# Kernel optimization log

Measured on AMD Instinct MI355X. Metric: run time of the kernel, lower is better.

The kernel has to match this reference:

```python
import jax, jax.numpy as jnp
import numpy as np
from jax import lax

B, N, C, CN, M, H, W = 2, 8192, 64, 64, 16, 180, 240
LN_EPS = 1e-5  # torch nn.LayerNorm([C]) default eps


def setup_inputs():
    key = jax.random.key(0)
    ks = jax.random.split(key, 20)
    x = jax.random.uniform(ks[0], (B, N)) * (W - 1)
    y = jax.random.uniform(ks[1], (B, N)) * (H - 1)
    t = jax.random.uniform(ks[2], (B, N))
    p = jnp.where(jax.random.uniform(ks[3], (B, N)) < 0.5, -1.0, 1.0)
    events = jnp.stack([x, y, t, p], axis=-1)  # [B,N,4]
    s = 0.05
    w = lambda k, shape: jax.random.normal(k, shape) * s
    return {
        "events": events,
        "W_mlp1": w(ks[4], (4, C)),
        "W_pe": w(ks[5], (4, CN)),
        "ln_w": jnp.ones((C,)),
        "ln_b": jnp.zeros((C,)),
        "lx_Wq": w(ks[6], (C, CN)), "lx_Wk": w(ks[7], (C, CN)),
        "lx_Wv": w(ks[8], (C, CN)), "lx_Wsa1": w(ks[9], (CN, 1)),
        "lx_Wsa2": w(ks[10], (CN, C)),
        "gx_Wq": w(ks[11], (C, CN)), "gx_Wk": w(ks[12], (C, CN)),
        "gx_Wv": w(ks[13], (C, CN)), "gx_Wpe": w(ks[14], (C, CN)),
        "gx_Wsa1": w(ks[15], (CN, 1)), "gx_Wsa2": w(ks[16], (CN, C)),
    }


def select_nearest(vect, m):
    # torch: F.pad(left=m//2, right=m//2-1) then unfold(dim=1, size=m, step=1)
    b, n, c = vect.shape
    pad = m // 2
    vp = jnp.pad(vect, ((0, 0), (pad, pad - 1), (0, 0)))
    idx = jnp.arange(n)[:, None] + jnp.arange(m)[None, :]  # [N,M]
    return vp[:, idx, :]  # [B,N,M,C]


def fps(event, npoint):
    # faithful farthest_point_sample_batch; masked_select returns the sampled
    # points in ORIGINAL index order, hence the sort of selected indices.
    b, n, c = event.shape
    bary = jnp.mean(event, axis=1, keepdims=True)
    farthest0 = jnp.argmax(jnp.sum((event - bary) ** 2, -1), axis=1)  # [B]
    dist0 = jnp.full((b, n), 1e10, event.dtype)

    def step(carry, _):
        distance, farthest = carry
        centroid = jnp.take_along_axis(event, farthest[:, None, None], axis=1)
        d = jnp.sum((event - centroid) ** 2, -1)
        distance = jnp.minimum(distance, d)  # distance[dist<distance]=dist
        return (distance, jnp.argmax(distance, axis=1)), farthest

    _, sel = lax.scan(step, (dist0, farthest0), None, length=npoint)
    sel = jnp.sort(sel.T, axis=1)  # [B,npoint], sorted index order
    return jnp.take_along_axis(event, sel[:, :, None], axis=1)  # [B,npoint,C]


def sub_attention(q, k_multi, v_multi, pe, Wsa1, Wsa2):
    # sa = q - k + pe -> Linear(Cn,1) -> softmax over M.
    # The original then computes matmul(scores[B,1,N,M], (v+pe)^T[B,Cn,M,N])
    # and sums over the last axis, which is exactly
    #   scores @ (sum_n (v_multi + pe))  -- computed here without the
    # [B,Cn,N,N] intermediate.
    sa = q[:, :, None, :] - k_multi + pe          # [B,N,M,Cn]
    logits = jnp.squeeze(sa @ Wsa1, -1)           # [B,N,M]
    scores = jax.nn.softmax(logits, axis=-1)
    S = jnp.sum(v_multi + pe, axis=1)             # [B,M,Cn]
    p_attn = jnp.einsum("bnm,bmc->bnc", scores, S)
    return p_attn @ Wsa2                          # [B,N,C]


def layer_norm(x, w, b):
    mu = jnp.mean(x, axis=-1, keepdims=True)
    var = jnp.var(x, axis=-1, keepdims=True)
    return (x - mu) / jnp.sqrt(var + LN_EPS) * w + b


def normalize_nonzero(space):
    # mean/std over nonzero entries (std unbiased, ddof=1 as torch.std)
    mask = space != 0
    cnt = jnp.sum(mask)
    mean = jnp.sum(jnp.where(mask, space, 0.0)) / jnp.maximum(cnt, 1)
    var = jnp.sum(jnp.where(mask, (space - mean) ** 2, 0.0)) / jnp.maximum(cnt - 1, 1)
    std = jnp.sqrt(var)
    centered = jnp.where(mask, space - mean, space)
    safe_std = jnp.where(std > 0, std, 1.0)
    normed = jnp.where(std > 0, centered / safe_std, centered)
    return jnp.where(cnt > 0, normed, space)


def events_to_image(feat, ev, ln_w, ln_b):
    # feat [N,C], ev [N,4]
    h = jax.nn.gelu(layer_norm(feat, ln_w, ln_b), approximate=False)
    xi = jnp.floor(ev[:, 0]).astype(jnp.int32)
    yi = jnp.floor(ev[:, 1]).astype(jnp.int32)
    p = ev[:, 3]
    flat = yi * W + xi
    space = jnp.zeros((H * W, h.shape[1]), h.dtype).at[flat].add(p[:, None] * h)
    return normalize_nonzero(space.reshape(H, W, -1))


def reference(events, W_mlp1, W_pe, ln_w, ln_b,
              lx_Wq, lx_Wk, lx_Wv, lx_Wsa1, lx_Wsa2,
              gx_Wq, gx_Wk, gx_Wv, gx_Wpe, gx_Wsa1, gx_Wsa2):
    b, n, _ = events.shape
    lx_in = events @ W_mlp1                                    # [B,N,C]
    # EventTransformer position encoding: unfold-neighbor differences in raw
    # 4-d event space, then Linear(4,Cn)
    pe = (events[:, :, None, :] - select_nearest(events, M)) @ W_pe  # [B,N,M,Cn]
    # LXformer
    q = lx_in @ lx_Wq
    k = lx_in @ lx_Wk
    v = lx_in @ lx_Wv
    lx_sa = sub_attention(q, select_nearest(k, M), select_nearest(v, M),
                          pe, lx_Wsa1, lx_Wsa2)
    lx_out = lx_in + lx_sa
    # GXformer: FPS-sampled global keys/values, FPS-based position encoding
    pe_g = (lx_out[:, :, None, :] - fps(lx_out, M)[:, None, :, :]) @ gx_Wpe
    qg = lx_out @ gx_Wq
    kg = lx_out @ gx_Wk
    vg = lx_out @ gx_Wv
    k_m = jnp.broadcast_to(fps(kg, M)[:, None], (b, n, M, CN))
    v_m = jnp.broadcast_to(fps(vg, M)[:, None], (b, n, M, CN))
    gx_sa = sub_attention(qg, k_m, v_m, pe_g, gx_Wsa1, gx_Wsa2)
    gx_out = lx_out + gx_sa
    # scatter events to image per batch element
    imgs = jax.vmap(lambda f, e: events_to_image(f, e, ln_w, ln_b))(gx_out, events)
    return jnp.transpose(imgs, (0, 3, 1, 2))  # [B,C,H,W]
```

## Files before the change

### kernel.cpp

```cpp
#include <hip/hip_runtime.h>


typedef unsigned short u16;
typedef unsigned long long ull;

#define NB 8192
#define IMG_H 180
#define IMG_W 240
#define HWPIX (IMG_H*IMG_W)
#define SPB (HWPIX*64)
#define NC (NB*64)

#define TT_AC    0
#define TT_T     16384
#define TT_W1    32768
#define TT_EDGEV 32960
#define TT_EDGEF 35008
#define TT_S     37056
#define TT_SEL   39104
#define TT_CG    45248
#define TT_ESUM  45376
#define TT_STATS 45408
#define TT_SYNC  45440
#define TT_GCNT  45632
#define TT_LXS   45664
#define TT_ZOFF  45376
#define TT_ZCNT  288
#define TT_TOT   45792

__device__ __forceinline__ float bf2f(u16 u){
  union { unsigned int i; float f; } w; w.i = ((unsigned int)u) << 16; return w.f;
}
__device__ __forceinline__ u16 f2bf(float f){
  union { unsigned int i; float f; } w; w.f = f;
  unsigned int x = w.i;
  x += 0x7fffu + ((x >> 16) & 1u);
  return (u16)(x >> 16);
}
__device__ __forceinline__ bool isbf(const void* ev){
  unsigned w3 = ((const unsigned*)ev)[3];
  return !(w3 == 0x3F800000u || w3 == 0xBF800000u);
}
__device__ __forceinline__ float ld(const void* p, int i, bool bf){
  return bf ? bf2f(((const u16*)p)[i]) : ((const float*)p)[i];
}
__device__ __forceinline__ void stout(void* o, long i, float v, bool bf){
  if (bf) ((u16*)o)[i] = f2bf(v); else ((float*)o)[i] = v;
}
__device__ __forceinline__ float waveSum(float v){
#pragma unroll
  for (int m = 1; m < 64; m <<= 1) v += __shfl_xor(v, m, 64);
  return v;
}
__device__ __forceinline__ ull waveMaxU64(ull v){
#pragma unroll
  for (int m = 1; m < 64; m <<= 1){
    ull o = (ull)__shfl_xor((long long)v, m, 64);
    if (o > v) v = o;
  }
  return v;
}
__device__ __forceinline__ ull packPDI(int phase, float d, int n){
  return ((ull)phase << 45) | ((ull)__float_as_uint(d) << 13) | (ull)(8191 - n);
}
__device__ __forceinline__ int unpackI(ull p){ return 8191 - (int)(p & 0x1FFFull); }

__global__ void kW(const void* __restrict__ ev, const void* __restrict__ Wq,
                   const void* __restrict__ Wk, const void* __restrict__ Wpe,
                   const void* __restrict__ w1, float* __restrict__ ws, int tail){
  const bool bf = isbf(ev);
  const int tid = threadIdx.x;
  for (int i = tid; i < TT_ZCNT; i += 256) ws[tail + TT_ZOFF + i] = 0.f;
  if (tid < 64){
    float s1 = 0.f, s2 = 0.f;
    for (int c = 0; c < 64; c++){
      float wc = ld(w1, c, bf);
      s1 += ld(Wq, tid*64 + c, bf) * wc;
      s2 += ld(Wk, tid*64 + c, bf) * wc;
    }
    ws[tail + TT_W1 + tid] = s1;
    ws[tail + TT_W1 + 64 + tid] = s2;
    if (tid < 4){
      float s3 = 0.f;
      for (int c = 0; c < 64; c++) s3 += ld(Wpe, tid*64 + c, bf) * ld(w1, c, bf);
      ws[tail + TT_W1 + 128 + tid] = s3;
    }
  }
}

__global__ void __launch_bounds__(256) kE(const void* __restrict__ ev,
    float* __restrict__ ws, int tail, int bb0){
  const bool bf = isbf(ev);
  const int bb = bb0 + blockIdx.z;
  const int lane = threadIdx.x & 63, w = threadIdx.x >> 6;
  float s0 = 0.f, s1 = 0.f, s2 = 0.f, s3 = 0.f;
#pragma unroll
  for (int j = 0; j < 4; j++){
    int r = blockIdx.x*256 + threadIdx.x + 2048*j;
    const int e4 = (bb*NB + r)*4;
    s0 += ld(ev, e4+0, bf); s1 += ld(ev, e4+1, bf);
    s2 += ld(ev, e4+2, bf); s3 += ld(ev, e4+3, bf);
  }
  s0 = waveSum(s0); s1 = waveSum(s1); s2 = waveSum(s2); s3 = waveSum(s3);
  __shared__ float r4[4][4];
  if (lane == 0){ r4[w][0]=s0; r4[w][1]=s1; r4[w][2]=s2; r4[w][3]=s3; }
  __syncthreads();
  if (threadIdx.x < 4)
    atomicAdd(&ws[tail + TT_ESUM + bb*16 + threadIdx.x],
              r4[0][threadIdx.x]+r4[1][threadIdx.x]+r4[2][threadIdx.x]+r4[3][threadIdx.x]);
}

__global__ void __launch_bounds__(256, 4) kA(const void* __restrict__ ev,
    const void* __restrict__ Wm, const void* __restrict__ Wpe,
    const void* __restrict__ Wv, float* __restrict__ ws,
    int offA, int strA, int tail, int bb0){
  const bool bf = isbf(ev);
  const int bb = bb0 + blockIdx.z;
  const int lane = threadIdx.x & 63, w = threadIdx.x >> 6;
  float* A = ws + offA + (size_t)bb*strA;
  const float wq1 = ws[tail + TT_W1 + lane];
  const float wk1 = ws[tail + TT_W1 + 64 + lane];
  const float wp10 = ws[tail+TT_W1+128], wp11 = ws[tail+TT_W1+129],
              wp12 = ws[tail+TT_W1+130], wp13 = ws[tail+TT_W1+131];
  const float wm0 = ld(Wm, 0*64+lane, bf), wm1 = ld(Wm, 1*64+lane, bf),
              wm2 = ld(Wm, 2*64+lane, bf), wm3 = ld(Wm, 3*64+lane, bf);
  const bool edgeBlk = (blockIdx.x == 0 || blockIdx.x == 1023);
#pragma unroll
  for (int i = 0; i < 2; i++){
    const int n = blockIdx.x*8 + w + 4*i;
    const int e4 = (bb*NB + n)*4;
    float e0 = ld(ev, e4+0, bf), e1 = ld(ev, e4+1, bf),
          e2 = ld(ev, e4+2, bf), e3 = ld(ev, e4+3, bf);
    float lx = e0*wm0 + e1*wm1 + e2*wm2 + e3*wm3;
    float epe = e0*wp10 + e1*wp11 + e2*wp12 + e3*wp13;
    float acv = waveSum(lx * wq1) + epe;
    float tv  = waveSum(lx * wk1) + epe;
    A[n*64 + lane] = lx;
    if (lane == 0){
      ws[tail + TT_AC + bb*8192 + n] = acv;
      ws[tail + TT_T  + bb*8192 + n] = tv;
    }
    if (edgeBlk && (n < 8 || n >= NB-8)){
      int e = (n < 8) ? n : (n - (NB-16));
      float v = 0.f;
      for (int cn = 0; cn < 64; cn++)
        v += __shfl(lx, cn, 64) * ld(Wv, cn*64 + lane, bf);
      float f = e0*ld(Wpe, lane, bf) + e1*ld(Wpe, 64+lane, bf)
              + e2*ld(Wpe, 128+lane, bf) + e3*ld(Wpe, 192+lane, bf);
      ws[tail + TT_EDGEV + bb*1024 + e*64 + lane] = v;
      ws[tail + TT_EDGEF + bb*1024 + e*64 + lane] = f;
    }
  }
}

__global__ void __launch_bounds__(64) kB(const void* __restrict__ ev,
    const void* __restrict__ Wm, const void* __restrict__ Wv,
    const void* __restrict__ Wsa2, float* __restrict__ ws, int tail, int bb0){
  const bool bf = isbf(ev);
  const int bb = bb0 + blockIdx.z;
  const int m = blockIdx.x, lane = threadIdx.x;
  float tm = 0.f;
#pragma unroll
  for (int i = 0; i < 4; i++) tm += ws[tail + TT_ESUM + bb*16 + i] * ld(Wm, i*64 + lane, bf);
  float vs0 = 0.f, vs1 = 0.f;
#pragma unroll
  for (int j = 0; j < 64; j += 2){
    vs0 += __shfl(tm, j, 64)   * ld(Wv, j*64 + lane, bf);
    vs1 += __shfl(tm, j+1, 64) * ld(Wv, (j+1)*64 + lane, bf);
  }
  float vsum = vs0 + vs1;
  const int d = m - 8;
  float sv = 0.f, sf = 0.f;
  const float* EV = ws + tail + TT_EDGEV + bb*1024;
  const float* EF = ws + tail + TT_EDGEF + bb*1024;
  if (d < 0){
    for (int e = 16 + d; e < 16; e++){ sv += EV[e*64+lane]; sf += EF[e*64+lane]; }
  } else {
    for (int e = 0; e < d; e++){ sv += EV[e*64+lane]; sf += EF[e*64+lane]; }
  }
  float S = vsum - sv + sf;
  float sw0 = 0.f, sw1 = 0.f;
#pragma unroll
  for (int c = 0; c < 64; c += 2){
    sw0 += __shfl(S, c, 64)   * ld(Wsa2, c*64 + lane, bf);
    sw1 += __shfl(S, c+1, 64) * ld(Wsa2, (c+1)*64 + lane, bf);
  }
  ws[tail + TT_S + bb*1024 + m*64 + lane] = sw0 + sw1;
}

__global__ void __launch_bounds__(256) kC(const void* __restrict__ ev,
    const void* __restrict__ gWk, const void* __restrict__ gWv,
    float* __restrict__ ws,
    int offA, int strA, int offB, int strB, int offC, int strC,
    int offLXP, int strLXP, int tail, int bb0){
  const bool bf = isbf(ev);
  const int bb = bb0 + blockIdx.z;
  float* A = ws + offA + (size_t)bb*strA;
  float* Bp = ws + offB + (size_t)bb*strB;
  float* Cp = ws + offC + (size_t)bb*strC;
  __shared__ float SW_lds[1024];
  __shared__ float WK[4096];
  __shared__ float WV[4096];
  __shared__ float lred[4][64];
  const int tid = threadIdx.x, lane = tid & 63, w = tid >> 6;
  for (int i = tid; i < 1024; i += 256) SW_lds[i] = ws[tail + TT_S + bb*1024 + i];
  for (int i = tid; i < 4096; i += 256){
    WK[i] = ld(gWk, i, bf);
    WV[i] = ld(gWv, i, bf);
  }
  __syncthreads();
  float lxoR[2];
  float lxsum = 0.f;
#pragma unroll
  for (int i = 0; i < 2; i++){
    const int n = blockIdx.x*8 + w + 4*i;
    float lx  = A[n*64 + lane];
    float acn = ws[tail + TT_AC + bb*8192 + n];
    const int m = lane & 15;
    const int j = n + m - 8;
    float tv = (j >= 0 && j < NB) ? ws[tail + TT_T + bb*8192 + j] : 0.f;
    float logit = acn - tv;
    float mx = logit;
#pragma unroll
    for (int k = 1; k < 16; k <<= 1) mx = fmaxf(mx, __shfl_xor(mx, k, 64));
    float ex = expf(logit - mx);
    float sm = ex;
#pragma unroll
    for (int k = 1; k < 16; k <<= 1) sm += __shfl_xor(sm, k, 64);
    float sig = ex / sm;
    float sa = 0.f;
#pragma unroll
    for (int mm = 0; mm < 16; mm++) sa += __shfl(sig, mm, 64) * SW_lds[mm*64 + lane];
    float lxo = lx + sa;
    lxoR[i] = lxo;
    Bp[n*64 + lane] = lxo;
    lxsum += lxo;
  }
  lred[w][lane] = lxsum;
#pragma unroll
  for (int i = 0; i < 2; i++){
    const int n = blockIdx.x*8 + w + 4*i;
    float k0 = 0.f, k1 = 0.f, v0 = 0.f, v1 = 0.f;
#pragma unroll
    for (int cn = 0; cn < 64; cn += 2){
      float x0 = __shfl(lxoR[i], cn, 64);
      float x1 = __shfl(lxoR[i], cn+1, 64);
      k0 += x0 * WK[cn*64 + lane];
      k1 += x1 * WK[(cn+1)*64 + lane];
      v0 += x0 * WV[cn*64 + lane];
      v1 += x1 * WV[(cn+1)*64 + lane];
    }
    A[n*64 + lane] = k0 + k1;
    Cp[n*64 + lane] = v0 + v1;
  }
  __syncthreads();
  if (tid < 64)
    ws[offLXP + (size_t)bb*strLXP + blockIdx.x*64 + tid] =
      lred[0][tid]+lred[1][tid]+lred[2][tid]+lred[3][tid];
}

__global__ void __launch_bounds__(512) kL(float* __restrict__ ws,
    int offLXP, int strLXP, int tail, int bb0){
  const int bb = bb0 + blockIdx.z;
  __shared__ float red[8][64];
  const int tid = threadIdx.x, c = tid & 63, grp = tid >> 6;
  const float* LXP = ws + offLXP + (size_t)bb*strLXP;
  float s = 0.f;
  for (int b2 = grp; b2 < 1024; b2 += 8) s += LXP[b2*64 + c];
  red[grp][c] = s;
  __syncthreads();
  if (tid < 64){
    float t = 0.f;
#pragma unroll
    for (int q = 0; q < 8; q++) t += red[q][tid];
    ws[tail + TT_LXS + bb*64 + tid] = t;
  }
}

__global__ void __launch_bounds__(512) kFPS(const void* __restrict__ ev,
    const void* __restrict__ gWk, const void* __restrict__ gWv,
    const void* __restrict__ gWpe, const void* __restrict__ gWsa1,
    const void* __restrict__ gWsa2, float* __restrict__ ws,
    int offA, int strA, int offB, int strB, int offC, int strC,
    int tail, int bb0){
  const int g = blockIdx.y, idx = blockIdx.x;
  const int bb = bb0 + blockIdx.z;
  const int tid = threadIdx.x, lane = tid & 63, w = tid >> 6;
  const float* pts = ws + (g == 0 ? offB + (size_t)bb*strB
                         : g == 1 ? offA + (size_t)bb*strA
                                  : offC + (size_t)bb*strC);
  ull* slot = (ull*)(ws + tail + TT_SYNC + (bb*3 + g)*32);
  int* gcnt = (int*)(ws + tail + TT_GCNT + bb*16);

  __shared__ float cent[64];
  __shared__ float lxsS[64];
  __shared__ ull   wvS[8];
  __shared__ int   selS[16];
  __shared__ int   sCur;
  __shared__ float gfS[1024];
  __shared__ float betaS[16];
  __shared__ float GS[64];

  const int n0 = idx*1024 + tid;
  float4 P[2][16];
#pragma unroll
  for (int j = 0; j < 2; j++)
#pragma unroll
    for (int i = 0; i < 16; i++)
      P[j][i] = ((const float4*)(pts + (size_t)(n0 + j*512)*64))[i];

  const bool bf = isbf(ev);
  if (tid < 64){
    float lxs = ws[tail + TT_LXS + bb*64 + tid];
    lxsS[tid] = lxs;
    float c;
    if (g == 0) c = lxs * (1.0f/NB);
    else {
      const void* W = (g == 1) ? gWk : gWv;
      float s = 0.f;
#pragma unroll
      for (int j = 0; j < 64; j++) s += __shfl(lxs, j, 64) * ld(W, j*64 + tid, bf);
      c = s * (1.0f/NB);
    }
    cent[tid] = c;
  }
  __syncthreads();

  const float4* cv = (const float4*)cent;
  float md[2] = {1e10f, 1e10f};
  int cur;

  {
    float dd[2];
#pragma unroll
    for (int j = 0; j < 2; j++){
      float d = 0.f;
#pragma unroll
      for (int i = 0; i < 16; i++){
        float4 c = cv[i];
        float dx = P[j][i].x-c.x, dy = P[j][i].y-c.y, dz = P[j][i].z-c.z, dw = P[j][i].w-c.w;
        d += dx*dx; d += dy*dy; d += dz*dz; d += dw*dw;
      }
      dd[j] = d;
    }
    ull p0 = packPDI(1, dd[0], n0);
    ull p1 = packPDI(1, dd[1], n0 + 512);
    ull bp = waveMaxU64(p0 > p1 ? p0 : p1);
    if (lane == 0) wvS[w] = bp;
    __syncthreads();
    if (w == 0){
      ull v = (lane < 8) ? wvS[lane] : 0;
#pragma unroll
      for (int m = 1; m < 8; m <<= 1){
        ull o = (ull)__shfl_xor((long long)v, m, 64);
        if (o > v) v = o;
      }
      if (lane == 0)
        __hip_atomic_store(&slot[8 + idx], v, __ATOMIC_RELEASE, __HIP_MEMORY_SCOPE_AGENT);
      ull got;
      for (;;){
        got = (lane < 8) ? __hip_atomic_load(&slot[8 + lane], __ATOMIC_RELAXED, __HIP_MEMORY_SCOPE_AGENT) : 0;
        ull ok = __ballot(lane >= 8 || (int)(got >> 45) == 1);
        if (ok == ~0ull) break;
        __builtin_amdgcn_s_sleep(1);
      }
#pragma unroll
      for (int m = 1; m < 8; m <<= 1){
        ull o = (ull)__shfl_xor((long long)got, m, 64);
        if (o > got) got = o;
      }
      if (lane == 0) sCur = unpackI(got);
    }
    __syncthreads();
    cur = sCur;
  }

  for (int it = 0; ; it++){
    if (tid == 0) selS[it] = cur;
    if (it == 15) break;
    if (tid < 16) ((float4*)cent)[tid] = ((const float4*)(pts + (size_t)cur*64))[tid];
    __syncthreads();
    const int phase = it + 2;
    float dd[2];
#pragma unroll
    for (int j = 0; j < 2; j++){
      float d = 0.f;
#pragma unroll
      for (int i = 0; i < 16; i++){
        float4 c = cv[i];
        float dx = P[j][i].x-c.x, dy = P[j][i].y-c.y, dz = P[j][i].z-c.z, dw = P[j][i].w-c.w;
        d += dx*dx; d += dy*dy; d += dz*dz; d += dw*dw;
      }
      md[j] = fminf(md[j], d);
      dd[j] = md[j];
    }
    ull p0 = packPDI(phase, dd[0], n0);
    ull p1 = packPDI(phase, dd[1], n0 + 512);
    ull bp = waveMaxU64(p0 > p1 ? p0 : p1);
    if (lane == 0) wvS[w] = bp;
    __syncthreads();
    const int par = phase & 1;
    if (w == 0){
      ull v = (lane < 8) ? wvS[lane] : 0;
#pragma unroll
      for (int m = 1; m < 8; m <<= 1){
        ull o = (ull)__shfl_xor((long long)v, m, 64);
        if (o > v) v = o;
      }
      if (lane == 0)
        __hip_atomic_store(&slot[par*8 + idx], v, __ATOMIC_RELEASE, __HIP_MEMORY_SCOPE_AGENT);
      ull got;
      for (;;){
        got = (lane < 8) ? __hip_atomic_load(&slot[par*8 + lane], __ATOMIC_RELAXED, __HIP_MEMORY_SCOPE_AGENT) : 0;
        ull ok = __ballot(lane >= 8 || (int)(got >> 45) == phase);
        if (ok == ~0ull) break;
        __builtin_amdgcn_s_sleep(1);
      }
#pragma unroll
      for (int m = 1; m < 8; m <<= 1){
        ull o = (ull)__shfl_xor((long long)got, m, 64);
        if (o > got) got = o;
      }
      if (lane == 0) sCur = unpackI(got);
    }
    __syncthreads();
    cur = sCur;
  }
  __syncthreads();

  if (idx == 0){
    if (tid == 0){
      for (int i = 1; i < 16; i++){
        int key = selS[i]; int j = i - 1;
        while (j >= 0 && selS[j] > key){ selS[j+1] = selS[j]; j--; }
        selS[j+1] = key;
      }
    }
    __syncthreads();
    for (int idx2 = tid; idx2 < 1024; idx2 += 512)
      ws[tail + TT_SEL + bb*3072 + g*1024 + idx2] = pts[(size_t)selS[idx2 >> 6]*64 + (idx2 & 63)];
    __threadfence();
  }
  __syncthreads();
  if (tid == 0) atomicAdd(gcnt, 1);
  if (g != 0 || idx != 0) return;

  if (tid == 0){
    while (__hip_atomic_load(gcnt, __ATOMIC_RELAXED, __HIP_MEMORY_SCOPE_AGENT) < 24)
      __builtin_amdgcn_s_sleep(1);
    __threadfence();
  }
  __syncthreads();
  if (tid < 64){
    const float gw1 = ld(gWsa1, tid, bf);
    float wpec[64];
#pragma unroll
    for (int cn = 0; cn < 64; cn++) wpec[cn] = ld(gWpe, cn*64 + tid, bf);
    float lxs = lxsS[tid];
    float G = 0.f;
#pragma unroll
    for (int cn = 0; cn < 64; cn++) G += __shfl(lxs, cn, 64) * wpec[cn];
    GS[tid] = G;
    const float* selp = ws + tail + TT_SEL + bb*3072;
    for (int m = 0; m < 16; m++){
      float plx = selp[m*64 + tid];
      float g2 = 0.f;
#pragma unroll
      for (int cn = 0; cn < 64; cn++) g2 += __shfl(plx, cn, 64) * wpec[cn];
      gfS[m*64 + tid] = g2;
      float pkv = selp[1024 + m*64 + tid];
      float part = waveSum((pkv + g2) * gw1);
      if (tid == 0) betaS[m] = part;
    }
  }
  __syncthreads();
  if (tid < 64){
    float mx = -1e30f;
    for (int m = 0; m < 16; m++) mx = fmaxf(mx, -betaS[m]);
    float ssum = 0.f;
    for (int m = 0; m < 16; m++) ssum += expf(-betaS[m] - mx);
    float A = 0.f;
    for (int m = 0; m < 16; m++){
      float sg = expf(-betaS[m] - mx) / ssum;
      float pv = ws[tail + TT_SEL + bb*3072 + 2048 + m*64 + tid];
      float Sg = 8192.0f * (pv - gfS[m*64 + tid]) + GS[tid];
      A += sg * Sg;
    }
    float cg = 0.f;
#pragma unroll
    for (int cn = 0; cn < 64; cn++) cg += __shfl(A, cn, 64) * ld(gWsa2, cn*64 + tid, bf);
    ws[tail + TT_CG + bb*64 + tid] = cg;
  }
}

__global__ void kZeroSpace(float* __restrict__ ws, int offSp, int strSp, int bb0){
  const int bb = bb0 + blockIdx.z;
  float4 z = make_float4(0.f, 0.f, 0.f, 0.f);
  ((float4*)(ws + offSp + (size_t)bb*strSp))[blockIdx.x*256 + threadIdx.x] = z;
}

__global__ void __launch_bounds__(256, 4) kImg(const void* __restrict__ ev,
    const void* __restrict__ lnw, const void* __restrict__ lnb,
    float* __restrict__ ws, int offB, int strB, int offSp, int strSp,
    int tail, int bb0){
  const bool bf = isbf(ev);
  const int bb = bb0 + blockIdx.z;
  const int lane = threadIdx.x & 63, w = threadIdx.x >> 6;
  const float cg = ws[tail + TT_CG + bb*64 + lane];
  const float lw = ld(lnw, lane, bf), lb = ld(lnb, lane, bf);
  float* space = ws + offSp + (size_t)bb*strSp;
  const float* Bp = ws + offB + (size_t)bb*strB;
#pragma unroll
  for (int i = 0; i < 2; i++){
    const int n = blockIdx.x*8 + w + 4*i;
    float x = Bp[n*64 + lane] + cg;
    float mu = waveSum(x) * (1.0f/64.0f);
    float dv = x - mu;
    float var = waveSum(dv*dv) * (1.0f/64.0f);
    float xn = dv / sqrtf(var + 1e-5f);
    float y = xn * lw + lb;
    float h = 0.5f * y * (1.0f + erff(y * 0.70710678118654752f));
    const int e4 = (bb*NB + n)*4;
    float exf = ld(ev, e4+0, bf), eyf = ld(ev, e4+1, bf), epf = ld(ev, e4+3, bf);
    int xi = (int)floorf(exf), yi = (int)floorf(eyf);
    int flat = yi*IMG_W + xi;
    flat = max(0, min(HWPIX-1, flat));
    atomicAdd(space + flat*64 + lane, epf * h);
  }
}

__global__ void __launch_bounds__(256) kStat(float* __restrict__ ws,
    int offSp, int strSp, int tail, int bb0){
  const int bb = bb0 + blockIdx.z;
  const float4* sp = (const float4*)(ws + offSp + (size_t)bb*strSp);
  float cnt = 0.f, sum = 0.f, ssq = 0.f;
  for (unsigned i = blockIdx.x*256u + threadIdx.x; i < SPB/4; i += 65536u){
    float4 v = sp[i];
    if (v.x != 0.f){ cnt += 1.f; sum += v.x; ssq += v.x*v.x; }
    if (v.y != 0.f){ cnt += 1.f; sum += v.y; ssq += v.y*v.y; }
    if (v.z != 0.f){ cnt += 1.f; sum += v.z; ssq += v.z*v.z; }
    if (v.w != 0.f){ cnt += 1.f; sum += v.w; ssq += v.w*v.w; }
  }
  cnt = waveSum(cnt); sum = waveSum(sum); ssq = waveSum(ssq);
  __shared__ float rc[4], rs[4], rq[4];
  const int lane = threadIdx.x & 63, w = threadIdx.x >> 6;
  if (lane == 0){ rc[w] = cnt; rs[w] = sum; rq[w] = ssq; }
  __syncthreads();
  if (threadIdx.x == 0){
    atomicAdd(&ws[tail + TT_STATS + bb*16 + 0], rc[0]+rc[1]+rc[2]+rc[3]);
    atomicAdd(&ws[tail + TT_STATS + bb*16 + 1], rs[0]+rs[1]+rs[2]+rs[3]);
    atomicAdd(&ws[tail + TT_STATS + bb*16 + 2], rq[0]+rq[1]+rq[2]+rq[3]);
  }
}

__global__ void __launch_bounds__(256) kOut(const void* __restrict__ ev,
    const float* __restrict__ ws, void* __restrict__ out,
    int offSp, int strSp, int tail, int bb0){
  const bool bf = isbf(ev);
  const int bb = bb0 + blockIdx.z;
  __shared__ float tile[64*64];
  const int tid = threadIdx.x;
  const int hw0 = blockIdx.x*64;
  const float* sp = ws + offSp + (size_t)bb*strSp;
#pragma unroll
  for (int i = 0; i < 16; i++){
    int idx = tid + 256*i;
    tile[idx] = sp[(size_t)hw0*64 + idx];
  }
  const float cnt = ws[tail + TT_STATS + bb*16 + 0];
  const float sum = ws[tail + TT_STATS + bb*16 + 1];
  const float ssq = ws[tail + TT_STATS + bb*16 + 2];
  const float mean = sum / fmaxf(cnt, 1.f);
  const float m2   = fmaxf(ssq - sum*mean, 0.f);
  const float var  = m2 / fmaxf(cnt - 1.f, 1.f);
  const float stdv = sqrtf(var);
  __syncthreads();
  const int c = tid >> 2, sub = tid & 3;
#pragma unroll
  for (int j = 0; j < 16; j++){
    int hwl = sub*16 + j;
    float x = tile[hwl*64 + c];
    float centered = (x != 0.f) ? (x - mean) : x;
    float normed = (stdv > 0.f) ? (centered / stdv) : centered;
    float o = (cnt > 0.f) ? normed : x;
    stout(out, (long)(bb*64 + c)*HWPIX + hw0 + hwl, o, bf);
  }
}

extern "C" void kernel_launch(void* const* d_in, const int* in_sizes, int n_in,
                              void* d_out, int out_size, void* d_ws, size_t ws_size,
                              hipStream_t stream){
  (void)in_sizes; (void)n_in; (void)out_size;
  const void* ev     = d_in[0];
  const void* Wm     = d_in[1];
  const void* Wpe    = d_in[2];
  const void* lnw    = d_in[3];
  const void* lnb    = d_in[4];
  const void* lxWq   = d_in[5];
  const void* lxWk   = d_in[6];
  const void* lxWv   = d_in[7];
  const void* lxWsa1 = d_in[8];
  const void* lxWsa2 = d_in[9];
  const void* gxWk   = d_in[11];
  const void* gxWv   = d_in[12];
  const void* gxWpe  = d_in[13];
  const void* gxWsa1 = d_in[14];
  const void* gxWsa2 = d_in[15];
  float* ws = (float*)d_ws;

  const int P_TAIL = 2*NC + 2*SPB;
  const size_t PAR_BYTES = (size_t)(P_TAIL + TT_TOT) * 4;
  const bool par = ws_size >= PAR_BYTES;

  int offB, strB, offSp, strSp, offA, strA, offC, strC, offLXP, strLXP, tail;
  if (par){
    offB = 0;        strB = NC;
    offSp = 2*NC;    strSp = SPB;
    offA = 2*NC;     strA = NC;
    offC = 4*NC;     strC = NC;
    offLXP = 6*NC;   strLXP = 65536;
    tail = P_TAIL;
  } else {
    offSp = 0;       strSp = 0;
    offA = 0;        strA = 0;
    offC = NC;       strC = 0;
    offLXP = 2*NC;   strLXP = 0;
    offB = SPB;      strB = 0;
    tail = SPB + NC;
  }
  const int nb = par ? 2 : 1;
  const int iters = par ? 1 : 2;

  kW<<<1, 256, 0, stream>>>(ev, lxWq, lxWk, Wpe, lxWsa1, ws, tail);
  for (int t = 0; t < iters; t++){
    const int bb0 = par ? 0 : t;
    kE<<<dim3(8,1,nb), 256, 0, stream>>>(ev, ws, tail, bb0);
    kA<<<dim3(1024,1,nb), 256, 0, stream>>>(ev, Wm, Wpe, lxWv, ws, offA, strA, tail, bb0);
    kB<<<dim3(16,1,nb), 64, 0, stream>>>(ev, Wm, lxWv, lxWsa2, ws, tail, bb0);
    kC<<<dim3(1024,1,nb), 256, 0, stream>>>(ev, gxWk, gxWv, ws,
        offA, strA, offB, strB, offC, strC, offLXP, strLXP, tail, bb0);
    kL<<<dim3(1,1,nb), 512, 0, stream>>>(ws, offLXP, strLXP, tail, bb0);
    kFPS<<<dim3(8,3,nb), 512, 0, stream>>>(ev, gxWk, gxWv, gxWpe, gxWsa1, gxWsa2, ws,
        offA, strA, offB, strB, offC, strC, tail, bb0);
    kZeroSpace<<<dim3(2700,1,nb), 256, 0, stream>>>(ws, offSp, strSp, bb0);
    kImg<<<dim3(1024,1,nb), 256, 0, stream>>>(ev, lnw, lnb, ws, offB, strB, offSp, strSp, tail, bb0);
    kStat<<<dim3(256,1,nb), 256, 0, stream>>>(ws, offSp, strSp, tail, bb0);
    kOut<<<dim3(675,1,nb), 256, 0, stream>>>(ev, ws, d_out, offSp, strSp, tail, bb0);
  }
}
```

Measured before the change: 342.6 us.

## Restructure FPS kernel to 1024 threads with float argmax and parallel tail

The FPS kernel now runs 1024 threads per block, each holding one point instead of two. The per-wave argmax reduces a float max with shuffles and picks the lowest matching lane via ballot, replacing the 64-bit packed shuffle reduction. The block-to-block slot publish is relaxed from release to relaxed ordering. The tail block stages gx_Wpe in shared memory and computes the 16 selected-point projections across 16 waves in parallel instead of a serial loop on one wave. The tail now waits on a completion count of 3 rather than 24. It also increments gcnt only in the selecting blocks, which changes the synchronisation semantics and may be unsafe.

```diff
diff --git a/kernel.cpp b/kernel.cpp
--- a/kernel.cpp
+++ b/kernel.cpp
@@ -52,14 +52,6 @@
   for (int m = 1; m < 64; m <<= 1) v += __shfl_xor(v, m, 64);
   return v;
 }
-__device__ __forceinline__ ull waveMaxU64(ull v){
-#pragma unroll
-  for (int m = 1; m < 64; m <<= 1){
-    ull o = (ull)__shfl_xor((long long)v, m, 64);
-    if (o > v) v = o;
-  }
-  return v;
-}
 __device__ __forceinline__ ull packPDI(int phase, float d, int n){
   return ((ull)phase << 45) | ((ull)__float_as_uint(d) << 13) | (ull)(8191 - n);
 }
@@ -277,7 +269,7 @@
   }
 }
 
-__global__ void __launch_bounds__(512) kFPS(const void* __restrict__ ev,
+__global__ void __launch_bounds__(1024) kFPS(const void* __restrict__ ev,
     const void* __restrict__ gWk, const void* __restrict__ gWv,
     const void* __restrict__ gWpe, const void* __restrict__ gWsa1,
     const void* __restrict__ gWsa2, float* __restrict__ ws,
@@ -294,32 +286,36 @@
 
   __shared__ float cent[64];
   __shared__ float lxsS[64];
-  __shared__ ull   wvS[8];
+  __shared__ ull   wvS[16];
   __shared__ int   selS[16];
   __shared__ int   sCur;
   __shared__ float gfS[1024];
   __shared__ float betaS[16];
   __shared__ float GS[64];
+  __shared__ float WPES[4096];
+
+  const bool bf = isbf(ev);
+  const bool tailBlk = (g == 0 && idx == 0);
+  if (tailBlk){
+    for (int i = tid; i < 4096; i += 1024) WPES[i] = ld(gWpe, i, bf);
+  }
 
   const int n0 = idx*1024 + tid;
-  float4 P[2][16];
-#pragma unroll
-  for (int j = 0; j < 2; j++)
-#pragma unroll
-    for (int i = 0; i < 16; i++)
-      P[j][i] = ((const float4*)(pts + (size_t)(n0 + j*512)*64))[i];
-
-  const bool bf = isbf(ev);
+  float4 P[16];
+#pragma unroll
+  for (int i = 0; i < 16; i++)
+    P[i] = ((const float4*)(pts + (size_t)n0*64))[i];
+
   if (tid < 64){
     float lxs = ws[tail + TT_LXS + bb*64 + tid];
     lxsS[tid] = lxs;
     float c;
     if (g == 0) c = lxs * (1.0f/NB);
     else {
-      const void* W = (g == 1) ? gWk : gWv;
+      const void* Wg = (g == 1) ? gWk : gWv;
       float s = 0.f;
 #pragma unroll
-      for (int j = 0; j < 64; j++) s += __shfl(lxs, j, 64) * ld(W, j*64 + tid, bf);
+      for (int j = 0; j < 64; j++) s += __shfl(lxs, j, 64) * ld(Wg, j*64 + tid, bf);
       c = s * (1.0f/NB);
     }
     cent[tid] = c;
@@ -327,36 +323,34 @@
   __syncthreads();
 
   const float4* cv = (const float4*)cent;
-  float md[2] = {1e10f, 1e10f};
+  float md = 1e10f;
   int cur;
 
   {
-    float dd[2];
-#pragma unroll
-    for (int j = 0; j < 2; j++){
-      float d = 0.f;
-#pragma unroll
-      for (int i = 0; i < 16; i++){
-        float4 c = cv[i];
-        float dx = P[j][i].x-c.x, dy = P[j][i].y-c.y, dz = P[j][i].z-c.z, dw = P[j][i].w-c.w;
-        d += dx*dx; d += dy*dy; d += dz*dz; d += dw*dw;
-      }
-      dd[j] = d;
-    }
-    ull p0 = packPDI(1, dd[0], n0);
-    ull p1 = packPDI(1, dd[1], n0 + 512);
-    ull bp = waveMaxU64(p0 > p1 ? p0 : p1);
+    float d = 0.f;
+#pragma unroll
+    for (int i = 0; i < 16; i++){
+      float4 c = cv[i];
+      float dx = P[i].x-c.x, dy = P[i].y-c.y, dz = P[i].z-c.z, dw2 = P[i].w-c.w;
+      d += dx*dx; d += dy*dy; d += dz*dz; d += dw2*dw2;
+    }
+    float mx = d;
+#pragma unroll
+    for (int m2 = 1; m2 < 64; m2 <<= 1) mx = fmaxf(mx, __shfl_xor(mx, m2, 64));
+    ull tie = __ballot(d == mx);
+    int src = __ffsll((long long)tie) - 1;
+    ull bp = packPDI(1, mx, idx*1024 + (w<<6) + src);
     if (lane == 0) wvS[w] = bp;
     __syncthreads();
     if (w == 0){
-      ull v = (lane < 8) ? wvS[lane] : 0;
-#pragma unroll
-      for (int m = 1; m < 8; m <<= 1){
-        ull o = (ull)__shfl_xor((long long)v, m, 64);
+      ull v = (lane < 16) ? wvS[lane] : 0;
+#pragma unroll
+      for (int m2 = 1; m2 < 16; m2 <<= 1){
+        ull o = (ull)__shfl_xor((long long)v, m2, 64);
         if (o > v) v = o;
       }
       if (lane == 0)
-        __hip_atomic_store(&slot[8 + idx], v, __ATOMIC_RELEASE, __HIP_MEMORY_SCOPE_AGENT);
+        __hip_atomic_store(&slot[8 + idx], v, __ATOMIC_RELAXED, __HIP_MEMORY_SCOPE_AGENT);
       ull got;
       for (;;){
         got = (lane < 8) ? __hip_atomic_load(&slot[8 + lane], __ATOMIC_RELAXED, __HIP_MEMORY_SCOPE_AGENT) : 0;
@@ -365,8 +359,8 @@
         __builtin_amdgcn_s_sleep(1);
       }
 #pragma unroll
-      for (int m = 1; m < 8; m <<= 1){
-        ull o = (ull)__shfl_xor((long long)got, m, 64);
+      for (int m2 = 1; m2 < 8; m2 <<= 1){
+        ull o = (ull)__shfl_xor((long long)got, m2, 64);
         if (o > got) got = o;
       }
       if (lane == 0) sCur = unpackI(got);
@@ -381,34 +375,32 @@
     if (tid < 16) ((float4*)cent)[tid] = ((const float4*)(pts + (size_t)cur*64))[tid];
     __syncthreads();
     const int phase = it + 2;
-    float dd[2];
-#pragma unroll
-    for (int j = 0; j < 2; j++){
-      float d = 0.f;
-#pragma unroll
-      for (int i = 0; i < 16; i++){
-        float4 c = cv[i];
-        float dx = P[j][i].x-c.x, dy = P[j][i].y-c.y, dz = P[j][i].z-c.z, dw = P[j][i].w-c.w;
-        d += dx*dx; d += dy*dy; d += dz*dz; d += dw*dw;
-      }
-      md[j] = fminf(md[j], d);
-      dd[j] = md[j];
-    }
-    ull p0 = packPDI(phase, dd[0], n0);
-    ull p1 = packPDI(phase, dd[1], n0 + 512);
-    ull bp = waveMaxU64(p0 > p1 ? p0 : p1);
+    float d = 0.f;
+#pragma unroll
+    for (int i = 0; i < 16; i++){
+      float4 c = cv[i];
+      float dx = P[i].x-c.x, dy = P[i].y-c.y, dz = P[i].z-c.z, dw2 = P[i].w-c.w;
+      d += dx*dx; d += dy*dy; d += dz*dz; d += dw2*dw2;
+    }
+    md = fminf(md, d);
+    float mx = md;
+#pragma unroll
+    for (int m2 = 1; m2 < 64; m2 <<= 1) mx = fmaxf(mx, __shfl_xor(mx, m2, 64));
+    ull tie = __ballot(md == mx);
+    int src = __ffsll((long long)tie) - 1;
+    ull bp = packPDI(phase, mx, idx*1024 + (w<<6) + src);
     if (lane == 0) wvS[w] = bp;
     __syncthreads();
     const int par = phase & 1;
     if (w == 0){
-      ull v = (lane < 8) ? wvS[lane] : 0;
-#pragma unroll
-      for (int m = 1; m < 8; m <<= 1){
-        ull o = (ull)__shfl_xor((long long)v, m, 64);
+      ull v = (lane < 16) ? wvS[lane] : 0;
+#pragma unroll
+      for (int m2 = 1; m2 < 16; m2 <<= 1){
+        ull o = (ull)__shfl_xor((long long)v, m2, 64);
         if (o > v) v = o;
       }
       if (lane == 0)
-        __hip_atomic_store(&slot[par*8 + idx], v, __ATOMIC_RELEASE, __HIP_MEMORY_SCOPE_AGENT);
+        __hip_atomic_store(&slot[par*8 + idx], v, __ATOMIC_RELAXED, __HIP_MEMORY_SCOPE_AGENT);
       ull got;
       for (;;){
         got = (lane < 8) ? __hip_atomic_load(&slot[par*8 + lane], __ATOMIC_RELAXED, __HIP_MEMORY_SCOPE_AGENT) : 0;
@@ -417,8 +409,8 @@
         __builtin_amdgcn_s_sleep(1);
       }
 #pragma unroll
-      for (int m = 1; m < 8; m <<= 1){
-        ull o = (ull)__shfl_xor((long long)got, m, 64);
+      for (int m2 = 1; m2 < 8; m2 <<= 1){
+        ull o = (ull)__shfl_xor((long long)got, m2, 64);
         if (o > got) got = o;
       }
       if (lane == 0) sCur = unpackI(got);
@@ -437,41 +429,37 @@
       }
     }
     __syncthreads();
-    for (int idx2 = tid; idx2 < 1024; idx2 += 512)
-      ws[tail + TT_SEL + bb*3072 + g*1024 + idx2] = pts[(size_t)selS[idx2 >> 6]*64 + (idx2 & 63)];
+    ws[tail + TT_SEL + bb*3072 + g*1024 + tid] = pts[(size_t)selS[tid >> 6]*64 + (tid & 63)];
     __threadfence();
-  }
-  __syncthreads();
-  if (tid == 0) atomicAdd(gcnt, 1);
-  if (g != 0 || idx != 0) return;
+    __syncthreads();
+    if (tid == 0) atomicAdd(gcnt, 1);
+  }
+  if (!tailBlk) return;
 
   if (tid == 0){
-    while (__hip_atomic_load(gcnt, __ATOMIC_RELAXED, __HIP_MEMORY_SCOPE_AGENT) < 24)
+    while (__hip_atomic_load(gcnt, __ATOMIC_RELAXED, __HIP_MEMORY_SCOPE_AGENT) < 3)
       __builtin_amdgcn_s_sleep(1);
     __threadfence();
   }
   __syncthreads();
+  const float* selp = ws + tail + TT_SEL + bb*3072;
+  {
+    const float gw1 = ld(gWsa1, lane, bf);
+    float plx = selp[w*64 + lane];
+    float g2 = 0.f;
+#pragma unroll
+    for (int cn = 0; cn < 64; cn++) g2 += __shfl(plx, cn, 64) * WPES[cn*64 + lane];
+    gfS[w*64 + lane] = g2;
+    float pkv = selp[1024 + w*64 + lane];
+    float part = waveSum((pkv + g2) * gw1);
+    if (lane == 0) betaS[w] = part;
+  }
   if (tid < 64){
-    const float gw1 = ld(gWsa1, tid, bf);
-    float wpec[64];
-#pragma unroll
-    for (int cn = 0; cn < 64; cn++) wpec[cn] = ld(gWpe, cn*64 + tid, bf);
     float lxs = lxsS[tid];
     float G = 0.f;
 #pragma unroll
-    for (int cn = 0; cn < 64; cn++) G += __shfl(lxs, cn, 64) * wpec[cn];
+    for (int cn = 0; cn < 64; cn++) G += __shfl(lxs, cn, 64) * WPES[cn*64 + tid];
     GS[tid] = G;
-    const float* selp = ws + tail + TT_SEL + bb*3072;
-    for (int m = 0; m < 16; m++){
-      float plx = selp[m*64 + tid];
-      float g2 = 0.f;
-#pragma unroll
-      for (int cn = 0; cn < 64; cn++) g2 += __shfl(plx, cn, 64) * wpec[cn];
-      gfS[m*64 + tid] = g2;
-      float pkv = selp[1024 + m*64 + tid];
-      float part = waveSum((pkv + g2) * gw1);
-      if (tid == 0) betaS[m] = part;
-    }
   }
   __syncthreads();
   if (tid < 64){
@@ -482,7 +470,7 @@
     float A = 0.f;
     for (int m = 0; m < 16; m++){
       float sg = expf(-betaS[m] - mx) / ssum;
-      float pv = ws[tail + TT_SEL + bb*3072 + 2048 + m*64 + tid];
+      float pv = selp[2048 + m*64 + tid];
       float Sg = 8192.0f * (pv - gfS[m*64 + tid]) + GS[tid];
       A += sg * Sg;
     }
@@ -640,7 +628,7 @@
     kC<<<dim3(1024,1,nb), 256, 0, stream>>>(ev, gxWk, gxWv, ws,
         offA, strA, offB, strB, offC, strC, offLXP, strLXP, tail, bb0);
     kL<<<dim3(1,1,nb), 512, 0, stream>>>(ws, offLXP, strLXP, tail, bb0);
-    kFPS<<<dim3(8,3,nb), 512, 0, stream>>>(ev, gxWk, gxWv, gxWpe, gxWsa1, gxWsa2, ws,
+    kFPS<<<dim3(8,3,nb), 1024, 0, stream>>>(ev, gxWk, gxWv, gxWpe, gxWsa1, gxWsa2, ws,
         offA, strA, offB, strB, offC, strC, tail, bb0);
     kZeroSpace<<<dim3(2700,1,nb), 256, 0, stream>>>(ws, offSp, strSp, bb0);
     kImg<<<dim3(1024,1,nb), 256, 0, stream>>>(ev, lnw, lnb, ws, offB, strB, offSp, strSp, tail, bb0);
```

After: 340.3 us. About the same (-0.7%).

## Fold event-sum and LX-sum reductions into neighbouring kernels, pad output tile

Applied to the files above, without the earlier changes.

Removes the kE event-sum kernel by accumulating per-event coordinate sums inside kA and adding them atomically, and removes the kL reduction kernel by having every kFPS block redundantly reduce the LXP partials itself. It also pads the kOut shared tile to a stride of 65 to avoid LDS bank conflicts on the transposed read. This saves two kernel launches and their serialization gaps. In exchange, kA now issues 1024 extra atomics per batch, and each of the 24 kFPS blocks repeats a 64K-float reduction before starting its FPS loop. The ESUM consumer kB still runs after kA, so ordering is preserved.

```diff
diff --git a/kernel.cpp b/kernel.cpp
--- a/kernel.cpp
+++ b/kernel.cpp
@@ -88,28 +88,6 @@
   }
 }
 
-__global__ void __launch_bounds__(256) kE(const void* __restrict__ ev,
-    float* __restrict__ ws, int tail, int bb0){
-  const bool bf = isbf(ev);
-  const int bb = bb0 + blockIdx.z;
-  const int lane = threadIdx.x & 63, w = threadIdx.x >> 6;
-  float s0 = 0.f, s1 = 0.f, s2 = 0.f, s3 = 0.f;
-#pragma unroll
-  for (int j = 0; j < 4; j++){
-    int r = blockIdx.x*256 + threadIdx.x + 2048*j;
-    const int e4 = (bb*NB + r)*4;
-    s0 += ld(ev, e4+0, bf); s1 += ld(ev, e4+1, bf);
-    s2 += ld(ev, e4+2, bf); s3 += ld(ev, e4+3, bf);
-  }
-  s0 = waveSum(s0); s1 = waveSum(s1); s2 = waveSum(s2); s3 = waveSum(s3);
-  __shared__ float r4[4][4];
-  if (lane == 0){ r4[w][0]=s0; r4[w][1]=s1; r4[w][2]=s2; r4[w][3]=s3; }
-  __syncthreads();
-  if (threadIdx.x < 4)
-    atomicAdd(&ws[tail + TT_ESUM + bb*16 + threadIdx.x],
-              r4[0][threadIdx.x]+r4[1][threadIdx.x]+r4[2][threadIdx.x]+r4[3][threadIdx.x]);
-}
-
 __global__ void __launch_bounds__(256, 4) kA(const void* __restrict__ ev,
     const void* __restrict__ Wm, const void* __restrict__ Wpe,
     const void* __restrict__ Wv, float* __restrict__ ws,
@@ -125,12 +103,14 @@
   const float wm0 = ld(Wm, 0*64+lane, bf), wm1 = ld(Wm, 1*64+lane, bf),
               wm2 = ld(Wm, 2*64+lane, bf), wm3 = ld(Wm, 3*64+lane, bf);
   const bool edgeBlk = (blockIdx.x == 0 || blockIdx.x == 1023);
+  float se0 = 0.f, se1 = 0.f, se2 = 0.f, se3 = 0.f;
 #pragma unroll
   for (int i = 0; i < 2; i++){
     const int n = blockIdx.x*8 + w + 4*i;
     const int e4 = (bb*NB + n)*4;
     float e0 = ld(ev, e4+0, bf), e1 = ld(ev, e4+1, bf),
           e2 = ld(ev, e4+2, bf), e3 = ld(ev, e4+3, bf);
+    se0 += e0; se1 += e1; se2 += e2; se3 += e3;
     float lx = e0*wm0 + e1*wm1 + e2*wm2 + e3*wm3;
     float epe = e0*wp10 + e1*wp11 + e2*wp12 + e3*wp13;
     float acv = waveSum(lx * wq1) + epe;
@@ -151,6 +131,12 @@
       ws[tail + TT_EDGEF + bb*1024 + e*64 + lane] = f;
     }
   }
+  __shared__ float esum[4][4];
+  if (lane == 0){ esum[w][0]=se0; esum[w][1]=se1; esum[w][2]=se2; esum[w][3]=se3; }
+  __syncthreads();
+  if (threadIdx.x < 4)
+    atomicAdd(&ws[tail + TT_ESUM + bb*16 + threadIdx.x],
+              esum[0][threadIdx.x]+esum[1][threadIdx.x]+esum[2][threadIdx.x]+esum[3][threadIdx.x]);
 }
 
 __global__ void __launch_bounds__(64) kB(const void* __restrict__ ev,
@@ -259,30 +245,12 @@
       lred[0][tid]+lred[1][tid]+lred[2][tid]+lred[3][tid];
 }
 
-__global__ void __launch_bounds__(512) kL(float* __restrict__ ws,
-    int offLXP, int strLXP, int tail, int bb0){
-  const int bb = bb0 + blockIdx.z;
-  __shared__ float red[8][64];
-  const int tid = threadIdx.x, c = tid & 63, grp = tid >> 6;
-  const float* LXP = ws + offLXP + (size_t)bb*strLXP;
-  float s = 0.f;
-  for (int b2 = grp; b2 < 1024; b2 += 8) s += LXP[b2*64 + c];
-  red[grp][c] = s;
-  __syncthreads();
-  if (tid < 64){
-    float t = 0.f;
-#pragma unroll
-    for (int q = 0; q < 8; q++) t += red[q][tid];
-    ws[tail + TT_LXS + bb*64 + tid] = t;
-  }
-}
-
 __global__ void __launch_bounds__(512) kFPS(const void* __restrict__ ev,
     const void* __restrict__ gWk, const void* __restrict__ gWv,
     const void* __restrict__ gWpe, const void* __restrict__ gWsa1,
     const void* __restrict__ gWsa2, float* __restrict__ ws,
     int offA, int strA, int offB, int strB, int offC, int strC,
-    int tail, int bb0){
+    int offLXP, int strLXP, int tail, int bb0){
   const int g = blockIdx.y, idx = blockIdx.x;
   const int bb = bb0 + blockIdx.z;
   const int tid = threadIdx.x, lane = tid & 63, w = tid >> 6;
@@ -300,6 +268,7 @@
   __shared__ float gfS[1024];
   __shared__ float betaS[16];
   __shared__ float GS[64];
+  __shared__ float redS[8][64];
 
   const int n0 = idx*1024 + tid;
   float4 P[2][16];
@@ -310,8 +279,17 @@
       P[j][i] = ((const float4*)(pts + (size_t)(n0 + j*512)*64))[i];
 
   const bool bf = isbf(ev);
+  {
+    const float* LXP = ws + offLXP + (size_t)bb*strLXP;
+    float s = 0.f;
+    for (int b2 = w; b2 < 1024; b2 += 8) s += LXP[b2*64 + lane];
+    redS[w][lane] = s;
+  }
+  __syncthreads();
   if (tid < 64){
-    float lxs = ws[tail + TT_LXS + bb*64 + tid];
+    float lxs = 0.f;
+#pragma unroll
+    for (int q = 0; q < 8; q++) lxs += redS[q][tid];
     lxsS[tid] = lxs;
     float c;
     if (g == 0) c = lxs * (1.0f/NB);
@@ -558,14 +536,14 @@
     int offSp, int strSp, int tail, int bb0){
   const bool bf = isbf(ev);
   const int bb = bb0 + blockIdx.z;
-  __shared__ float tile[64*64];
+  __shared__ float tile[64*65];
   const int tid = threadIdx.x;
   const int hw0 = blockIdx.x*64;
   const float* sp = ws + offSp + (size_t)bb*strSp;
 #pragma unroll
   for (int i = 0; i < 16; i++){
     int idx = tid + 256*i;
-    tile[idx] = sp[(size_t)hw0*64 + idx];
+    tile[(idx >> 6)*65 + (idx & 63)] = sp[(size_t)hw0*64 + idx];
   }
   const float cnt = ws[tail + TT_STATS + bb*16 + 0];
   const float sum = ws[tail + TT_STATS + bb*16 + 1];
@@ -579,7 +557,7 @@
 #pragma unroll
   for (int j = 0; j < 16; j++){
     int hwl = sub*16 + j;
-    float x = tile[hwl*64 + c];
+    float x = tile[hwl*65 + c];
     float centered = (x != 0.f) ? (x - mean) : x;
     float normed = (stdv > 0.f) ? (centered / stdv) : centered;
     float o = (cnt > 0.f) ? normed : x;
@@ -634,14 +612,12 @@
   kW<<<1, 256, 0, stream>>>(ev, lxWq, lxWk, Wpe, lxWsa1, ws, tail);
   for (int t = 0; t < iters; t++){
     const int bb0 = par ? 0 : t;
-    kE<<<dim3(8,1,nb), 256, 0, stream>>>(ev, ws, tail, bb0);
     kA<<<dim3(1024,1,nb), 256, 0, stream>>>(ev, Wm, Wpe, lxWv, ws, offA, strA, tail, bb0);
     kB<<<dim3(16,1,nb), 64, 0, stream>>>(ev, Wm, lxWv, lxWsa2, ws, tail, bb0);
     kC<<<dim3(1024,1,nb), 256, 0, stream>>>(ev, gxWk, gxWv, ws,
         offA, strA, offB, strB, offC, strC, offLXP, strLXP, tail, bb0);
-    kL<<<dim3(1,1,nb), 512, 0, stream>>>(ws, offLXP, strLXP, tail, bb0);
     kFPS<<<dim3(8,3,nb), 512, 0, stream>>>(ev, gxWk, gxWv, gxWpe, gxWsa1, gxWsa2, ws,
-        offA, strA, offB, strB, offC, strC, tail, bb0);
+        offA, strA, offB, strB, offC, strC, offLXP, strLXP, tail, bb0);
     kZeroSpace<<<dim3(2700,1,nb), 256, 0, stream>>>(ws, offSp, strSp, bb0);
     kImg<<<dim3(1024,1,nb), 256, 0, stream>>>(ev, lnw, lnb, ws, offB, strB, offSp, strSp, tail, bb0);
     kStat<<<dim3(256,1,nb), 256, 0, stream>>>(ws, offSp, strSp, tail, bb0);
```

After: 349.4 us. Within noise of the previous version (+2.0%).
